# Performance work log

Measured on AMD Instinct MI355X. Metric: run time of the kernel, lower is better.

The kernel has to match this reference:

```python
import jax, jax.numpy as jnp
import numpy as np

B, S, D, H = 4, 2048, 1024, 16
HD = D // H


def setup_inputs() -> dict:
    key = jax.random.key(0)
    ks = jax.random.split(key, 9)
    s = 1.0 / np.sqrt(D)
    return {
        "x": jax.random.normal(ks[0], (B, S, D), dtype=jnp.float32),
        "wq": jax.random.uniform(ks[1], (D, D), jnp.float32, -s, s),
        "bq": jax.random.uniform(ks[2], (D,), jnp.float32, -s, s),
        "wk": jax.random.uniform(ks[3], (D, D), jnp.float32, -s, s),
        "bk": jax.random.uniform(ks[4], (D,), jnp.float32, -s, s),
        "wv": jax.random.uniform(ks[5], (D, D), jnp.float32, -s, s),
        "bv": jax.random.uniform(ks[6], (D,), jnp.float32, -s, s),
        "wo": jax.random.uniform(ks[7], (D, D), jnp.float32, -s, s),
        "bo": jax.random.uniform(ks[8], (D,), jnp.float32, -s, s),
    }


def reference(x, wq, bq, wk, bk, wv, bv, wo, bo):
    b, s, _ = x.shape
    # QKV projections, split into heads: [B, H, S, HD]
    q = (x @ wq + bq).reshape(b, s, H, HD).transpose(0, 2, 1, 3)
    k = (x @ wk + bk).reshape(b, s, H, HD).transpose(0, 2, 1, 3)
    v = (x @ wv + bv).reshape(b, s, H, HD).transpose(0, 2, 1, 3)
    # Full score matrix [B, H, S, S] as the original does
    scores = jnp.einsum("bhqd,bhkd->bhqk", q, k) / jnp.sqrt(jnp.float32(HD))
    attn = jax.nn.softmax(scores, axis=-1)  # dropout is identity in eval mode
    ctx = jnp.einsum("bhqk,bhkd->bhqd", attn, v)
    ctx = ctx.transpose(0, 2, 1, 3).reshape(b, s, D)
    return ctx @ wo + bo
```

## Files before the change

kernel.cpp:

```cpp
#include <hip/hip_runtime.h>
#include <hip/hip_bf16.h>
#include <stdint.h>

#define B_  4
#define S_  2048
#define D_  1024
#define H_  16
#define HD_ 64

using bf16x8 = __attribute__((ext_vector_type(8))) short;
using f32x2  = __attribute__((ext_vector_type(2))) float;
using f32x4  = __attribute__((ext_vector_type(4))) float;
using f32x8  = __attribute__((ext_vector_type(8))) float;
using f32x16 = __attribute__((ext_vector_type(16))) float;
using i32x2  = __attribute__((ext_vector_type(2))) int;
using i32x4  = __attribute__((ext_vector_type(4))) int;

#define QSCALE 0.18033688011112042f

#if __has_builtin(__builtin_amdgcn_exp2f)
#define EXP2F(x) __builtin_amdgcn_exp2f(x)
#else
#define EXP2F(x) exp2f(x)
#endif

__device__ __forceinline__ short f2b(float f) {
  union { __hip_bfloat16 h; short s; } u;
  u.h = __float2bfloat16(f);
  return u.s;
}

__device__ __forceinline__ unsigned cvtpk(float lo, float hi) {
  unsigned r;
  asm("v_cvt_pk_bf16_f32 %0, %1, %2" : "=v"(r) : "v"(lo), "v"(hi));
  return r;
}

__device__ __forceinline__ float max3f(float a, float b, float c) {
  float d;
  asm("v_max3_f32 %0, %1, %2, %3" : "=v"(d) : "v"(a), "v"(b), "v"(c));
  return d;
}

__device__ __forceinline__ void g2lds16(const void* g, void* l) {
  __builtin_amdgcn_global_load_lds(
      (const __attribute__((address_space(1))) uint32_t*)(uintptr_t)g,
      (__attribute__((address_space(3))) uint32_t*)(uint32_t)(uintptr_t)l,
      16, 0, 0);
}


__global__ __launch_bounds__(256) void k_cvt_x(const float* __restrict__ x,
                                               short* __restrict__ xb, int n8) {
  int i = blockIdx.x * 256 + threadIdx.x;
  if (i >= n8) return;
  const float4* xp = (const float4*)x;
  float4 a = xp[2 * i], b = xp[2 * i + 1];
  bf16x8 o;
  o[0] = f2b(a.x); o[1] = f2b(a.y); o[2] = f2b(a.z); o[3] = f2b(a.w);
  o[4] = f2b(b.x); o[5] = f2b(b.y); o[6] = f2b(b.z); o[7] = f2b(b.w);
  ((bf16x8*)xb)[i] = o;
}

__global__ __launch_bounds__(256) void k_cvt_w(
    const float* __restrict__ wq, const float* __restrict__ wk,
    const float* __restrict__ wv, const float* __restrict__ wo,
    short* __restrict__ wqkvT, short* __restrict__ woT) {
  __shared__ float tile[32][33];
  int wi = blockIdx.z;
  const float* src = wi == 0 ? wq : wi == 1 ? wk : wi == 2 ? wv : wo;
  float scale = (wi == 0) ? QSCALE : 1.0f;
  short* dst = wi < 3 ? wqkvT + (size_t)wi * D_ * D_ : woT;
  int n0 = blockIdx.x * 32, k0 = blockIdx.y * 32;
  int tx = threadIdx.x, ty = threadIdx.y;
#pragma unroll
  for (int j = 0; j < 4; ++j)
    tile[ty + j * 8][tx] = src[(size_t)(k0 + ty + j * 8) * D_ + n0 + tx];
  __syncthreads();
#pragma unroll
  for (int j = 0; j < 4; ++j)
    dst[(size_t)(n0 + ty + j * 8) * D_ + k0 + tx] = f2b(tile[tx][ty + j * 8] * scale);
}

__global__ void k_cvt_b(const float* __restrict__ bq, const float* __restrict__ bk,
                        const float* __restrict__ bv, float* __restrict__ biasqkv) {
  int i = blockIdx.x * 256 + threadIdx.x;
  if (i >= 3 * D_) return;
  float v = (i < D_) ? bq[i] * QSCALE : (i < 2 * D_) ? bk[i - D_] : bv[i - 2 * D_];
  biasqkv[i] = v;
}


template <int MODE>
__global__ __launch_bounds__(256, 2) void k_gemm(
    const short* __restrict__ A, const short* __restrict__ Bt,
    const float* __restrict__ bias, float* __restrict__ outF,
    short* __restrict__ Qo, short* __restrict__ Ko, short* __restrict__ Vo) {
  constexpr int K = 1024;
  __shared__ short Als[128 * 64];
  __shared__ short Bls[128 * 64];
  const int tid = threadIdx.x;
  const int wave = tid >> 6, lane = tid & 63;
  const int wr = wave >> 1, wc = wave & 1;
  const int l15 = lane & 15, l4 = lane >> 4;
  const int rowBase = blockIdx.x * 128;
  const int colBase = blockIdx.y * 128;

  f32x4 zero4 = {0.f, 0.f, 0.f, 0.f};
  f32x4 acc[4][4];
#pragma unroll
  for (int m = 0; m < 4; ++m)
#pragma unroll
    for (int n = 0; n < 4; ++n) acc[m][n] = zero4;

  for (int kt = 0; kt < K; kt += 64) {
#pragma unroll
    for (int i = 0; i < 4; ++i) {
      int c = i * 256 + tid;
      int r = c >> 3;
      int ko = ((c & 7) * 8) ^ ((r & 7) << 3);
      g2lds16(A + (size_t)(rowBase + r) * K + kt + ko, &Als[(i * 256 + wave * 64) * 8]);
      g2lds16(Bt + (size_t)(colBase + r) * K + kt + ko, &Bls[(i * 256 + wave * 64) * 8]);
    }
    __syncthreads();
#pragma unroll
    for (int kk = 0; kk < 2; ++kk) {
      bf16x8 af[4], bfr[4];
#pragma unroll
      for (int m = 0; m < 4; ++m) {
        int r = wr * 64 + m * 16 + l15;
        af[m] = *(const bf16x8*)&Als[r * 64 + ((kk * 32 + l4 * 8) ^ ((r & 7) << 3))];
      }
#pragma unroll
      for (int n = 0; n < 4; ++n) {
        int r = wc * 64 + n * 16 + l15;
        bfr[n] = *(const bf16x8*)&Bls[r * 64 + ((kk * 32 + l4 * 8) ^ ((r & 7) << 3))];
      }
#pragma unroll
      for (int m = 0; m < 4; ++m)
#pragma unroll
        for (int n = 0; n < 4; ++n)
          acc[m][n] = __builtin_amdgcn_mfma_f32_16x16x32_bf16(af[m], bfr[n], acc[m][n], 0, 0, 0);
    }
    __syncthreads();
  }

#pragma unroll
  for (int n = 0; n < 4; ++n) {
    int n_g = colBase + wc * 64 + n * 16 + l15;
    float bia = bias[n_g];
#pragma unroll
    for (int m = 0; m < 4; ++m) {
#pragma unroll
      for (int r = 0; r < 4; ++r) {
        int m_g = rowBase + wr * 64 + m * 16 + l4 * 4 + r;
        float v = acc[m][n][r] + bia;
        if constexpr (MODE == 0) {
          int p = n_g >> 10, dm = n_g & 1023, h = dm >> 6, hd = dm & 63;
          int b = m_g >> 11, s = m_g & 2047;
          short* dst = p == 0 ? Qo : p == 1 ? Ko : Vo;
          size_t idx;
          if (p == 2) idx = ((size_t)((b * H_ + h) * HD_ + hd)) * S_ + s;
          else        idx = ((size_t)((b * H_ + h) * S_ + s)) * HD_ + hd;
          dst[idx] = f2b(v);
        } else {
          outF[(size_t)m_g * D_ + n_g] = v;
        }
      }
    }
  }
}


__global__ __launch_bounds__(256, 4) void k_attn2(
    const short* __restrict__ Q, const short* __restrict__ K,
    const short* __restrict__ Vt, short* __restrict__ ctx) {
  __shared__ short Kls[2][64 * 64];
  __shared__ short Vls[2][64 * 64];
  const int bh = blockIdx.y;
  const int q0 = blockIdx.x * 128;
  const int tid = threadIdx.x, wave = tid >> 6, lane = tid & 63;
  const int l31 = lane & 31, hi = lane >> 5;
  const short* Qb = Q + (size_t)bh * S_ * HD_;
  const short* Kb = K + (size_t)bh * S_ * HD_;
  const short* Vb = Vt + (size_t)bh * HD_ * S_;

  bf16x8 qf[4];
#pragma unroll
  for (int ks = 0; ks < 4; ++ks)
    qf[ks] = *(const bf16x8*)&Qb[(size_t)(q0 + wave * 32 + l31) * HD_ + ks * 16 + hi * 8];

  f32x16 ctxa[2];
#pragma unroll
  for (int n = 0; n < 2; ++n)
#pragma unroll
    for (int i = 0; i < 16; ++i) ctxa[n][i] = 0.f;
  float m = -1e30f, lsum = 0.f;

#define STAGE(kv0, b)                                                          \
  {                                                                            \
    _Pragma("unroll") for (int i = 0; i < 2; ++i) {                            \
      int c = i * 256 + tid;                                                   \
      int r = c >> 3;                                                          \
      int off = ((c & 7) * 8) ^ ((r & 7) << 3);                                \
      g2lds16(Kb + (size_t)((kv0) + r) * HD_ + off,                            \
              &Kls[b][(i * 256 + wave * 64) * 8]);                             \
      g2lds16(Vb + (size_t)r * S_ + (kv0) + off,                               \
              &Vls[b][(i * 256 + wave * 64) * 8]);                             \
    }                                                                          \
  }

  STAGE(0, 0);
  int buf = 0;
#pragma unroll 1
  for (int t = 0; t < S_ / 64; ++t) {
    __syncthreads();
    STAGE((((t + 1) & 31) * 64), (buf ^ 1));

    f32x16 sa[2];
    __builtin_amdgcn_s_setprio(1);
#pragma unroll
    for (int tt = 0; tt < 2; ++tt) {
#pragma unroll
      for (int i = 0; i < 16; ++i) sa[tt][i] = 0.f;
#pragma unroll
      for (int ks = 0; ks < 4; ++ks) {
        int r = tt * 32 + l31;
        bf16x8 kf = *(const bf16x8*)&Kls[buf][r * 64 + ((ks * 16 + hi * 8) ^ ((r & 7) << 3))];
        sa[tt] = __builtin_amdgcn_mfma_f32_32x32x16_bf16(kf, qf[ks], sa[tt], 0, 0, 0);
      }
    }
    __builtin_amdgcn_s_setprio(0);

    float t0[8], t1[4];
#pragma unroll
    for (int i = 0; i < 8; ++i) t0[i] = max3f(sa[0][i], sa[0][i + 8], sa[1][i]);
#pragma unroll
    for (int i = 0; i < 4; ++i) t1[i] = max3f(t0[i], t0[i + 4], sa[1][i + 8]);
    float u0 = max3f(t1[0], t1[2], sa[1][12]);
    float u1 = max3f(t1[1], t1[3], sa[1][13]);
    float z = max3f(u0, u1, sa[1][14]);
    z = fmaxf(z, sa[1][15]);
    float mx = fmaxf(z, __shfl_xor(z, 32));

    if (!__all(mx - m <= 8.f)) {
      float mnew = fmaxf(m, mx);
      float corr = EXP2F(m - mnew);
      lsum *= corr;
      ctxa[0] *= corr;
      ctxa[1] *= corr;
      m = mnew;
    }
#pragma unroll
    for (int tt = 0; tt < 2; ++tt) {
      f32x16 dd = sa[tt] - m;
#pragma unroll
      for (int i = 0; i < 16; ++i) sa[tt][i] = EXP2F(dd[i]);
    }
    f32x16 vs = sa[0] + sa[1];
    f32x8 a8 = __builtin_shufflevector(vs, vs, 0, 1, 2, 3, 4, 5, 6, 7)
             + __builtin_shufflevector(vs, vs, 8, 9, 10, 11, 12, 13, 14, 15);
    f32x4 a4 = __builtin_shufflevector(a8, a8, 0, 1, 2, 3)
             + __builtin_shufflevector(a8, a8, 4, 5, 6, 7);
    f32x2 a2 = __builtin_shufflevector(a4, a4, 0, 1)
             + __builtin_shufflevector(a4, a4, 2, 3);
    float rs = a2[0] + a2[1];
    rs += __shfl_xor(rs, 32);
    lsum += rs;

    __builtin_amdgcn_s_setprio(1);
#pragma unroll
    for (int ks = 0; ks < 4; ++ks) {
      int tt = ks >> 1, s1 = ks & 1;
      unsigned x0 = cvtpk(sa[tt][8 * s1 + 0], sa[tt][8 * s1 + 1]);
      unsigned x1 = cvtpk(sa[tt][8 * s1 + 2], sa[tt][8 * s1 + 3]);
      unsigned y0 = cvtpk(sa[tt][8 * s1 + 4], sa[tt][8 * s1 + 5]);
      unsigned y1 = cvtpk(sa[tt][8 * s1 + 6], sa[tt][8 * s1 + 7]);
      i32x2 r0 = __builtin_amdgcn_permlane32_swap((int)x0, (int)y0, false, false);
      i32x2 r1 = __builtin_amdgcn_permlane32_swap((int)x1, (int)y1, false, false);
      union { i32x4 i; bf16x8 h; } pu;
      pu.i = (i32x4){r0[0], r1[0], r0[1], r1[1]};
#pragma unroll
      for (int nn = 0; nn < 2; ++nn) {
        int r = nn * 32 + l31;
        bf16x8 vf = *(const bf16x8*)&Vls[buf][r * 64 + ((ks * 16 + hi * 8) ^ ((r & 7) << 3))];
        ctxa[nn] = __builtin_amdgcn_mfma_f32_32x32x16_bf16(vf, pu.h, ctxa[nn], 0, 0, 0);
      }
    }
    __builtin_amdgcn_s_setprio(0);
    buf ^= 1;
  }

  __syncthreads();
  short* Pw = &Kls[0][0] + wave * 2048;
  float inv = 1.0f / lsum;
#pragma unroll
  for (int tt = 0; tt < 2; ++tt)
#pragma unroll
    for (int g = 0; g < 4; ++g) {
      unsigned d0 = cvtpk(ctxa[tt][4 * g + 0] * inv, ctxa[tt][4 * g + 1] * inv);
      unsigned d1 = cvtpk(ctxa[tt][4 * g + 2] * inv, ctxa[tt][4 * g + 3] * inv);
      int hd0 = tt * 32 + g * 8 + hi * 4;
      *(i32x2*)((char*)Pw + l31 * 128 + ((hd0 * 2) ^ ((l31 & 7) << 3))) =
          (i32x2){(int)d0, (int)d1};
    }
  __syncthreads();
  const int b = bh >> 4, h = bh & 15;
#pragma unroll
  for (int p = 0; p < 8; ++p) {
    int c = p * 64 + lane;
    int q = c >> 4, s8 = c & 15;
    i32x2 v = *(const i32x2*)((const char*)Pw + q * 128 + ((s8 * 8) ^ ((q & 7) << 3)));
    int row = q0 + wave * 32 + q;
    *(i32x2*)&ctx[((size_t)(b * S_ + row)) * D_ + h * HD_ + s8 * 4] = v;
  }
}


extern "C" void kernel_launch(void* const* d_in, const int* in_sizes, int n_in,
                              void* d_out, int out_size, void* d_ws, size_t ws_size,
                              hipStream_t stream) {
  const float* x  = (const float*)d_in[0];
  const float* wq = (const float*)d_in[1];
  const float* bq = (const float*)d_in[2];
  const float* wk = (const float*)d_in[3];
  const float* bk = (const float*)d_in[4];
  const float* wv = (const float*)d_in[5];
  const float* bv = (const float*)d_in[6];
  const float* wo = (const float*)d_in[7];
  const float* bo = (const float*)d_in[8];
  float* out = (float*)d_out;

  char* ws = (char*)d_ws;
  short* xb    = (short*)(ws);
  short* wqkvT = (short*)(ws + (16 << 20));
  short* woT   = (short*)(ws + (22 << 20));
  float* biasq = (float*)(ws + (24 << 20));
  short* Qb    = (short*)(ws + (25 << 20));
  short* Kb    = (short*)(ws + (41 << 20));
  short* Vb    = (short*)(ws + (57 << 20));

  k_cvt_x<<<dim3(4096), dim3(256), 0, stream>>>(x, xb, (B_ * S_ * D_) / 8);
  k_cvt_w<<<dim3(32, 32, 4), dim3(32, 8), 0, stream>>>(wq, wk, wv, wo, wqkvT, woT);
  k_cvt_b<<<dim3(12), dim3(256), 0, stream>>>(bq, bk, bv, biasq);

  k_gemm<0><<<dim3(64, 24), dim3(256), 0, stream>>>(xb, wqkvT, biasq,
                                                    (float*)nullptr, Qb, Kb, Vb);
  k_attn2<<<dim3(S_ / 128, B_ * H_), dim3(256), 0, stream>>>(Qb, Kb, Vb, xb );
  k_gemm<1><<<dim3(64, 8), dim3(256), 0, stream>>>(xb, woT, bo, out,
                                                   nullptr, nullptr, nullptr);
}
```

Baseline: 197.2 us.

## Replace QKV projection GEMM with 256x256 8-wave double-buffered pipelined kernel

Adds a new QKV projection kernel with 256x256 tiles and 8 waves. It uses double-buffered LDS, direct global-to-LDS loads with XOR swizzling, and an interleaved schedule of loads and MFMA quarters using barriers, waitcnt and setprio. It also remaps block indices for better L2 reuse. The aim is to raise MFMA utilization and hide memory latency, at the cost of large LDS use, more registers and a fragile hand-tuned schedule. The old templated GEMM is kept only for the output projection.

```diff
diff --git a/kernel.cpp b/kernel.cpp
--- a/kernel.cpp
+++ b/kernel.cpp
@@ -91,11 +91,141 @@
 }
 
 
+#define READ_A(b, mb)                                                          \
+  _Pragma("unroll") for (int mm = 0; mm < 2; ++mm)                             \
+      _Pragma("unroll") for (int ks = 0; ks < 2; ++ks) {                       \
+    int rr = wm * 128 + ((mb) + mm) * 16 + l15;                                \
+    af[mm][ks] = *(const bf16x8*)&lds[b][0][rr * 64 +                          \
+                  ((ks * 32 + l4 * 8) ^ ((rr & 7) << 3))];                     \
+  }
+
+#define READ_B(b)                                                              \
+  _Pragma("unroll") for (int nn = 0; nn < 4; ++nn)                             \
+      _Pragma("unroll") for (int ks = 0; ks < 2; ++ks) {                       \
+    int rr = wn * 64 + nn * 16 + l15;                                          \
+    bfr[nn][ks] = *(const bf16x8*)&lds[b][1][rr * 64 +                         \
+                   ((ks * 32 + l4 * 8) ^ ((rr & 7) << 3))];                    \
+  }
+
+#define MFMA_Q(mb)                                                             \
+  _Pragma("unroll") for (int ks = 0; ks < 2; ++ks)                             \
+      _Pragma("unroll") for (int mm = 0; mm < 2; ++mm)                         \
+          _Pragma("unroll") for (int nn = 0; nn < 4; ++nn)                     \
+    acc[(mb) + mm][nn] = __builtin_amdgcn_mfma_f32_16x16x32_bf16(              \
+        af[mm][ks], bfr[nn][ks], acc[(mb) + mm][nn], 0, 0, 0);
+
+#define GBAR __builtin_amdgcn_s_barrier()
+#define LGKM0                                                                  \
+  do {                                                                         \
+    asm volatile("s_waitcnt lgkmcnt(0)" ::: "memory");                         \
+    __builtin_amdgcn_sched_barrier(0);                                         \
+  } while (0)
+#define PRIO1 __builtin_amdgcn_s_setprio(1)
+#define PRIO0 __builtin_amdgcn_s_setprio(0)
+#define VMC(n) asm volatile("s_waitcnt vmcnt(" #n ")" ::: "memory")
+
+__global__ __launch_bounds__(512, 2) void k_gemm8(
+    const short* __restrict__ A, const short* __restrict__ Bt,
+    const float* __restrict__ bias,
+    short* __restrict__ Qo, short* __restrict__ Ko, short* __restrict__ Vo) {
+  __shared__ short lds[2][2][256 * 64];
+  const int tid = threadIdx.x;
+  const int wave = tid >> 6, lane = tid & 63;
+  const int wm = wave >> 2, wn = wave & 3;
+  const int l15 = lane & 15, l4 = lane >> 4;
+
+  int swz = (blockIdx.x & 7) * 48 + (blockIdx.x >> 3);
+  int bx = swz / 12, by = swz % 12;
+  const int rowBase = bx * 256, colBase = by * 256;
+
+  const short* Ablk = A + (size_t)rowBase * 1024;
+  const short* Bblk = Bt + (size_t)colBase * 1024;
+
+  auto STG = [&](const short* g, int kt, int r0, short* lb) {
+    int rr = tid >> 3, c8 = tid & 7;
+    g2lds16(g + (size_t)(r0 + rr) * 1024 + kt * 64 + ((c8 ^ (rr & 7)) << 3),
+            lb + r0 * 64 + wave * 512);
+  };
+  short* L0A = &lds[0][0][0]; short* L0B = &lds[0][1][0];
+  short* L1A = &lds[1][0][0]; short* L1B = &lds[1][1][0];
+
+  f32x4 acc[8][4];
+#pragma unroll
+  for (int m = 0; m < 8; ++m)
+#pragma unroll
+    for (int n = 0; n < 4; ++n) acc[m][n] = (f32x4){0.f, 0.f, 0.f, 0.f};
+
+  STG(Bblk, 0, 0, L0B);  STG(Bblk, 0, 64, L0B);
+  STG(Bblk, 0, 128, L0B); STG(Bblk, 0, 192, L0B);
+  STG(Ablk, 0, 0, L0A);  STG(Ablk, 0, 64, L0A);
+  STG(Ablk, 0, 128, L0A); STG(Ablk, 0, 192, L0A);
+  STG(Bblk, 1, 0, L1B);  STG(Bblk, 1, 64, L1B);
+  STG(Bblk, 1, 128, L1B); STG(Bblk, 1, 192, L1B);
+  STG(Ablk, 1, 0, L1A);  STG(Ablk, 1, 128, L1A);
+  VMC(6);
+  GBAR;
+
+#pragma unroll 1
+  for (int i = 0; i < 8; ++i) {
+    const int u = 2 * i + 1, v = 2 * i + 2, w = 2 * i + 3;
+    const bool pre = (i < 7);
+    bf16x8 af[2][2], bfr[4][2];
+    READ_B(0); READ_A(0, 0);
+    STG(Ablk, u, 64, L1A); STG(Ablk, u, 192, L1A);
+    GBAR; LGKM0; PRIO1; MFMA_Q(0); PRIO0; GBAR;
+    READ_A(0, 2);
+    if (pre) { STG(Bblk, v, 0, L0B); STG(Bblk, v, 64, L0B); }
+    GBAR; LGKM0; PRIO1; MFMA_Q(2); PRIO0; GBAR;
+    READ_A(0, 4);
+    if (pre) { STG(Bblk, v, 128, L0B); STG(Bblk, v, 192, L0B); }
+    GBAR; LGKM0; PRIO1; MFMA_Q(4); PRIO0; GBAR;
+    READ_A(0, 6);
+    if (pre) { STG(Ablk, v, 0, L0A); STG(Ablk, v, 128, L0A); }
+    GBAR; LGKM0; PRIO1; MFMA_Q(6); PRIO0;
+    if (pre) VMC(6); else VMC(0);
+    GBAR;
+    READ_B(1); READ_A(1, 0);
+    if (pre) { STG(Ablk, v, 64, L0A); STG(Ablk, v, 192, L0A); }
+    GBAR; LGKM0; PRIO1; MFMA_Q(0); PRIO0; GBAR;
+    READ_A(1, 2);
+    if (pre) { STG(Bblk, w, 0, L1B); STG(Bblk, w, 64, L1B); }
+    GBAR; LGKM0; PRIO1; MFMA_Q(2); PRIO0; GBAR;
+    READ_A(1, 4);
+    if (pre) { STG(Bblk, w, 128, L1B); STG(Bblk, w, 192, L1B); }
+    GBAR; LGKM0; PRIO1; MFMA_Q(4); PRIO0; GBAR;
+    READ_A(1, 6);
+    if (pre) { STG(Ablk, w, 0, L1A); STG(Ablk, w, 128, L1A); }
+    GBAR; LGKM0; PRIO1; MFMA_Q(6); PRIO0;
+    if (pre) VMC(6); else VMC(0);
+    GBAR;
+  }
+
+#pragma unroll
+  for (int n = 0; n < 4; ++n) {
+    int n_g = colBase + wn * 64 + n * 16 + l15;
+    float bia = bias[n_g];
+    int p = n_g >> 10, dm = n_g & 1023, h = dm >> 6, hd = dm & 63;
+    short* dst = p == 0 ? Qo : p == 1 ? Ko : Vo;
+#pragma unroll
+    for (int m = 0; m < 8; ++m) {
+#pragma unroll
+      for (int r = 0; r < 4; ++r) {
+        int m_g = rowBase + wm * 128 + m * 16 + l4 * 4 + r;
+        int b = m_g >> 11, s = m_g & 2047;
+        float vv = acc[m][n][r] + bia;
+        size_t idx = (p == 2) ? ((size_t)((b * H_ + h) * HD_ + hd)) * S_ + s
+                              : ((size_t)((b * H_ + h) * S_ + s)) * HD_ + hd;
+        dst[idx] = f2b(vv);
+      }
+    }
+  }
+}
+
+
 template <int MODE>
 __global__ __launch_bounds__(256, 2) void k_gemm(
     const short* __restrict__ A, const short* __restrict__ Bt,
-    const float* __restrict__ bias, float* __restrict__ outF,
-    short* __restrict__ Qo, short* __restrict__ Ko, short* __restrict__ Vo) {
+    const float* __restrict__ bias, float* __restrict__ outF) {
   constexpr int K = 1024;
   __shared__ short Als[128 * 64];
   __shared__ short Bls[128 * 64];
@@ -154,18 +284,7 @@
 #pragma unroll
       for (int r = 0; r < 4; ++r) {
         int m_g = rowBase + wr * 64 + m * 16 + l4 * 4 + r;
-        float v = acc[m][n][r] + bia;
-        if constexpr (MODE == 0) {
-          int p = n_g >> 10, dm = n_g & 1023, h = dm >> 6, hd = dm & 63;
-          int b = m_g >> 11, s = m_g & 2047;
-          short* dst = p == 0 ? Qo : p == 1 ? Ko : Vo;
-          size_t idx;
-          if (p == 2) idx = ((size_t)((b * H_ + h) * HD_ + hd)) * S_ + s;
-          else        idx = ((size_t)((b * H_ + h) * S_ + s)) * HD_ + hd;
-          dst[idx] = f2b(v);
-        } else {
-          outF[(size_t)m_g * D_ + n_g] = v;
-        }
+        outF[(size_t)m_g * D_ + n_g] = acc[m][n][r] + bia;
       }
     }
   }
@@ -344,9 +463,7 @@
   k_cvt_w<<<dim3(32, 32, 4), dim3(32, 8), 0, stream>>>(wq, wk, wv, wo, wqkvT, woT);
   k_cvt_b<<<dim3(12), dim3(256), 0, stream>>>(bq, bk, bv, biasq);
 
-  k_gemm<0><<<dim3(64, 24), dim3(256), 0, stream>>>(xb, wqkvT, biasq,
-                                                    (float*)nullptr, Qb, Kb, Vb);
+  k_gemm8<<<dim3(384), dim3(512), 0, stream>>>(xb, wqkvT, biasq, Qb, Kb, Vb);
   k_attn2<<<dim3(S_ / 128, B_ * H_), dim3(256), 0, stream>>>(Qb, Kb, Vb, xb );
-  k_gemm<1><<<dim3(64, 8), dim3(256), 0, stream>>>(xb, woT, bo, out,
-                                                   nullptr, nullptr, nullptr);
-}
+  k_gemm<1><<<dim3(64, 8), dim3(256), 0, stream>>>(xb, woT, bo, out);
+}
```

New measurement: 223.1 us. +13.1%, slower.
